# Optimization experiments

Hardware: AMD Instinct MI355X
Metric: run time of the kernel (lower is better)

The kernel has to match this reference:

```python
import jax, jax.numpy as jnp
import numpy as np

NUM_CLASSES = 1203
NO_OBJECT = NUM_CLASSES - 1  # CONSTANTS.NO_OBJECT_LABEL
BZ, N = 64, 100


def _cxcywh_to_xyxy(b):
    cx, cy, w, h = b[..., 0], b[..., 1], b[..., 2], b[..., 3]
    return jnp.stack([cx - w / 2, cy - h / 2, cx + w / 2, cy + h / 2], axis=-1)


def _pairwise_iou_np(a, b):
    # a: [M,4] xyxy, b: [K,4] xyxy -> [M,K]
    area_a = (a[:, 2] - a[:, 0]) * (a[:, 3] - a[:, 1])
    area_b = (b[:, 2] - b[:, 0]) * (b[:, 3] - b[:, 1])
    lt = np.maximum(a[:, None, :2], b[None, :, :2])
    rb = np.minimum(a[:, None, 2:], b[None, :, 2:])
    wh = np.clip(rb - lt, 0.0, None)
    inter = wh[..., 0] * wh[..., 1]
    union = area_a[:, None] + area_b[None, :] - inter
    return inter / np.maximum(union, 1e-9)


def _lsa(cost):
    # Exact Hungarian (Jonker-Volgenant / e-maxx potentials), square cost [n,n].
    # Returns col_of_row: assigned column (target) for each row (prediction).
    n = cost.shape[0]
    INF = 1e18
    u = np.zeros(n + 1)
    v = np.zeros(n + 1)
    p = np.zeros(n + 1, dtype=np.int64)   # p[j] = row matched to column j (1-indexed)
    way = np.zeros(n + 1, dtype=np.int64)
    for i in range(1, n + 1):
        p[0] = i
        j0 = 0
        minv = np.full(n + 1, INF)
        used = np.zeros(n + 1, dtype=bool)
        while True:
            used[j0] = True
            i0 = p[j0]
            cur = cost[i0 - 1] - u[i0] - v[1:]
            unused = ~used[1:]
            improve = unused & (cur < minv[1:])
            minv[1:][improve] = cur[improve]
            way[1:][improve] = j0
            masked = np.where(unused, minv[1:], INF)
            j1 = int(np.argmin(masked)) + 1
            delta = masked[j1 - 1]
            u[p[used]] += delta
            v[used] -= delta
            minv[1:][unused] -= delta
            j0 = j1
            if p[j0] == 0:
                break
        while j0 != 0:
            j1 = way[j0]
            p[j0] = p[j1]
            j0 = j1
    col_of_row = np.zeros(n, dtype=np.int64)
    for j in range(1, n + 1):
        col_of_row[p[j] - 1] = j - 1
    return col_of_row


def _cxcywh_to_xyxy_np(b):
    cx, cy, w, h = b[..., 0], b[..., 1], b[..., 2], b[..., 3]
    return np.stack([cx - w / 2, cy - h / 2, cx + w / 2, cy + h / 2], axis=-1)


def _hungarian_match(labs, lab_preds, bbox, bbox_preds):
    # numpy matcher, mirrors HungarianMatcher.forward (no_grad).
    bz = labs.shape[0]
    # stable softmax over classes
    z = lab_preds - lab_preds.max(axis=-1, keepdims=True)
    e = np.exp(z)
    probs = e / e.sum(axis=-1, keepdims=True)  # [bz,N,C]
    gt_idx = np.zeros(labs.shape, dtype=np.int64)
    for b in range(bz):
        cost_class = -probs[b][:, labs[b]]                                   # [N,N]
        cost_bbox = np.abs(bbox_preds[b][:, None, :] - bbox[b][None, :, :]).sum(-1)
        iou = _pairwise_iou_np(_cxcywh_to_xyxy_np(bbox_preds[b]),
                               _cxcywh_to_xyxy_np(bbox[b]))
        C = cost_class + cost_bbox + (1.0 - iou)
        gt_idx[b] = _lsa(C.astype(np.float64))  # row_ind == arange(N) for square C
    return gt_idx


def _elementwise_iou(a, b):
    # a, b: [...,4] xyxy, paired IoU
    lt = jnp.maximum(a[..., :2], b[..., :2])
    rb = jnp.minimum(a[..., 2:], b[..., 2:])
    wh = jnp.clip(rb - lt, 0.0)
    inter = wh[..., 0] * wh[..., 1]
    area_a = (a[..., 2] - a[..., 0]) * (a[..., 3] - a[..., 1])
    area_b = (b[..., 2] - b[..., 0]) * (b[..., 3] - b[..., 1])
    union = area_a + area_b - inter
    return inter / jnp.maximum(union, 1e-9)


def _detr_loss(labs, lab_preds, bbox, bbox_preds, gt_idx):
    # Re-gather GT by matching (pred side is identity since row_ind=arange(N)).
    new_labs = jnp.take_along_axis(labs, gt_idx, axis=1)                  # [bz,N]
    new_bbox = jnp.take_along_axis(bbox, gt_idx[..., None], axis=1)      # [bz,N,4]
    probs = jax.nn.softmax(lab_preds, axis=-1)
    pred_cls = jnp.argmax(probs, axis=-1)
    mask = (new_labs != NO_OBJECT) & (new_labs == pred_cls)              # [bz,N]
    # classification term: mean over ALL bz*N entries of -p[gt_label]
    loss_label = -jnp.take_along_axis(probs, new_labs[..., None], axis=2).squeeze(-1)
    loss_label = loss_label.mean()
    cnt = mask.sum()
    # L1: torch's bbox[mask] flattens -> .sum(-1).mean() is a plain SUM of |diff|
    l1 = jnp.sum(jnp.abs(new_bbox - bbox_preds) * mask[..., None])
    # IoU loss: mean over masked boxes of (1 - iou)
    iou = _elementwise_iou(_cxcywh_to_xyxy(new_bbox), _cxcywh_to_xyxy(bbox_preds))
    liou = jnp.sum((1.0 - iou) * mask) / jnp.maximum(cnt, 1)
    return loss_label + l1 + liou


def setup_inputs() -> dict:
    key = jax.random.key(0)
    k1, k2, k3, k4 = jax.random.split(key, 4)
    labs = jax.random.randint(k1, (BZ, N), 0, NUM_CLASSES, dtype=jnp.int64)
    lab_preds = jax.random.normal(k2, (BZ, N, NUM_CLASSES), dtype=jnp.float32)
    bbox = jax.random.uniform(k3, (BZ, N, 4), dtype=jnp.float32)
    bbox_preds = jax.random.uniform(k4, (BZ, N, 4), dtype=jnp.float32)
    return {"labs": labs, "lab_preds": lab_preds, "bbox": bbox, "bbox_preds": bbox_preds}


def reference(labs, lab_preds, bbox, bbox_preds):
    gt_idx = _hungarian_match(np.asarray(labs),
                              np.asarray(lab_preds, dtype=np.float64),
                              np.asarray(bbox, dtype=np.float64),
                              np.asarray(bbox_preds, dtype=np.float64))
    return _detr_loss(labs, lab_preds, bbox, bbox_preds, jnp.asarray(gt_idx))
```

## Files before the change

### kernel.cpp

```cpp
#include <hip/hip_runtime.h>
#include <hip/hip_bf16.h>
#include <math.h>
#include <float.h>

#define BZ 64
#define NQ 100
#define NCLS 1203
#define NO_OBJ 1202
constexpr double HUNG_INF = 1e18;
#define KINF 0xC3ABC16D674EC800ull

__device__ inline double readlane_f64(double x, int l) {
  int lo = __builtin_amdgcn_readlane(__double2loint(x), l);
  int hi = __builtin_amdgcn_readlane(__double2hiint(x), l);
  return __hiloint2double(hi, lo);
}

template <int CTRL>
__device__ inline unsigned dpp_mov_u32(unsigned x) {
  return (unsigned)__builtin_amdgcn_update_dpp((int)x, (int)x, CTRL, 0xF, 0xF, false);
}
__device__ inline unsigned umin32(unsigned a, unsigned b) { return a < b ? a : b; }

__device__ inline unsigned wave_min_u32(unsigned x) {
  x = umin32(x, dpp_mov_u32<0xB1>(x));
  x = umin32(x, dpp_mov_u32<0x4E>(x));
  x = umin32(x, dpp_mov_u32<0x141>(x));
  x = umin32(x, dpp_mov_u32<0x128>(x));
  unsigned a = (unsigned)__builtin_amdgcn_readlane((int)x, 0);
  unsigned c = (unsigned)__builtin_amdgcn_readlane((int)x, 16);
  unsigned d = (unsigned)__builtin_amdgcn_readlane((int)x, 32);
  unsigned e = (unsigned)__builtin_amdgcn_readlane((int)x, 48);
  return umin32(umin32(a, c), umin32(d, e));
}

__device__ inline unsigned long long f64_key(double d) {
  long long b = __double_as_longlong(d);
  long long m = (b >> 63) | (long long)0x8000000000000000ll;
  return (unsigned long long)(b ^ m);
}
__device__ inline double key_to_f64(unsigned long long k) {
  long long kk = (long long)k;
  long long m = ((~kk) >> 63) | (long long)0x8000000000000000ll;
  return __longlong_as_double(kk ^ m);
}

__global__ __launch_bounds__(64) void rowstats_kernel(
    const float* __restrict__ lab_preds,
    double* __restrict__ rowmax, double* __restrict__ rowsum,
    float* __restrict__ mxf, float* __restrict__ sf, int* __restrict__ amx) {
  const int r = blockIdx.x;
  const int t = threadIdx.x;
  const float* row = lab_preds + (size_t)r * NCLS;
  float fm = -FLT_MAX; int am = NCLS;
  for (int c = t; c < NCLS; c += 64) {
    float vv = row[c];
    if (vv > fm) { fm = vv; am = c; }
  }
#pragma unroll
  for (int off = 32; off; off >>= 1) {
    float ov = __shfl_xor(fm, off); int oi = __shfl_xor(am, off);
    if (ov > fm || (ov == fm && oi < am)) { fm = ov; am = oi; }
  }
  const double mx = (double)fm;
  double s = 0.0;
  for (int c = t; c < NCLS; c += 64) s += exp((double)row[c] - mx);
#pragma unroll
  for (int off = 32; off; off >>= 1) s += __shfl_xor(s, off);
  float sfl = 0.0f;
  for (int c = t; c < NCLS; c += 64) sfl += expf(row[c] - fm);
#pragma unroll
  for (int off = 32; off; off >>= 1) sfl += __shfl_xor(sfl, off);
  if (t == 0) {
    rowmax[r] = mx; rowsum[r] = s;
    mxf[r] = fm; sf[r] = sfl; amx[r] = am;
  }
}

__global__ __launch_bounds__(64) void match_kernel(
    const int* __restrict__ labs, const float* __restrict__ lab_preds,
    const float* __restrict__ bbox, const float* __restrict__ bbox_preds,
    const double* __restrict__ rowmax, const double* __restrict__ rowsum,
    int* __restrict__ gt_idx) {
  __shared__ double2 Csh2[NQ * 64];
  __shared__ int labs_sh[NQ];
  __shared__ int rowclaim[NQ];
  __shared__ double pxy[NQ][4], txy[NQ][4], pcx[NQ][4], tcx[NQ][4];
  __shared__ double areaP[NQ], areaT[NQ], rmax[NQ], rsum[NQ];

  const int b = blockIdx.x;
  const int lane = threadIdx.x;

  for (int j = lane; j < NQ; j += 64) {
    labs_sh[j] = labs[b * NQ + j];
    const float* tb = bbox + ((size_t)b * NQ + j) * 4;
    double cx = tb[0], cy = tb[1], w = tb[2], h = tb[3];
    tcx[j][0] = cx; tcx[j][1] = cy; tcx[j][2] = w; tcx[j][3] = h;
    double x1 = cx - w * 0.5, y1 = cy - h * 0.5, x2 = cx + w * 0.5, y2 = cy + h * 0.5;
    txy[j][0] = x1; txy[j][1] = y1; txy[j][2] = x2; txy[j][3] = y2;
    areaT[j] = (x2 - x1) * (y2 - y1);
    const float* pb = bbox_preds + ((size_t)b * NQ + j) * 4;
    cx = pb[0]; cy = pb[1]; w = pb[2]; h = pb[3];
    pcx[j][0] = cx; pcx[j][1] = cy; pcx[j][2] = w; pcx[j][3] = h;
    x1 = cx - w * 0.5; y1 = cy - h * 0.5; x2 = cx + w * 0.5; y2 = cy + h * 0.5;
    pxy[j][0] = x1; pxy[j][1] = y1; pxy[j][2] = x2; pxy[j][3] = y2;
    areaP[j] = (x2 - x1) * (y2 - y1);
    rmax[j] = rowmax[b * NQ + j];
    rsum[j] = rowsum[b * NQ + j];
  }
  for (int r = lane; r < NQ; r += 64) rowclaim[r] = -1;
  __syncthreads();

  for (int i = 0; i < NQ; ++i) {
    double cA, cB = 0.0;
    {
      const int j = lane;
      double pc = exp((double)lab_preds[((size_t)b * NQ + i) * NCLS + labs_sh[j]] - rmax[i]) / rsum[i];
      double cb = fabs(pcx[i][0] - tcx[j][0]) + fabs(pcx[i][1] - tcx[j][1])
                + fabs(pcx[i][2] - tcx[j][2]) + fabs(pcx[i][3] - tcx[j][3]);
      double ltx = fmax(pxy[i][0], txy[j][0]);
      double lty = fmax(pxy[i][1], txy[j][1]);
      double rbx = fmin(pxy[i][2], txy[j][2]);
      double rby = fmin(pxy[i][3], txy[j][3]);
      double inter = fmax(rbx - ltx, 0.0) * fmax(rby - lty, 0.0);
      double uni = areaP[i] + areaT[j] - inter;
      double iou = inter / fmax(uni, 1e-9);
      cA = -pc + cb + (1.0 - iou);
    }
    if (lane + 64 < NQ) {
      const int j = lane + 64;
      double pc = exp((double)lab_preds[((size_t)b * NQ + i) * NCLS + labs_sh[j]] - rmax[i]) / rsum[i];
      double cb = fabs(pcx[i][0] - tcx[j][0]) + fabs(pcx[i][1] - tcx[j][1])
                + fabs(pcx[i][2] - tcx[j][2]) + fabs(pcx[i][3] - tcx[j][3]);
      double ltx = fmax(pxy[i][0], txy[j][0]);
      double lty = fmax(pxy[i][1], txy[j][1]);
      double rbx = fmin(pxy[i][2], txy[j][2]);
      double rby = fmin(pxy[i][3], txy[j][3]);
      double inter = fmax(rbx - ltx, 0.0) * fmax(rby - lty, 0.0);
      double uni = areaP[i] + areaT[j] - inter;
      double iou = inter / fmax(uni, 1e-9);
      cB = -pc + cb + (1.0 - iou);
    }
    Csh2[i * 64 + lane] = make_double2(cA, cB);
  }
  __syncthreads();

  const bool has1 = (lane + 65 <= NQ);

  double mn0 = DBL_MAX, mn1 = DBL_MAX; int ar0 = 0, ar1 = 0;
  for (int i = 0; i < NQ; ++i) {
    double2 cd = Csh2[i * 64 + lane];
    if (cd.x < mn0) { mn0 = cd.x; ar0 = i; }
    if (has1 && cd.y < mn1) { mn1 = cd.y; ar1 = i; }
  }
  double v0 = mn0, v1 = has1 ? mn1 : 0.0;
  double u0 = 0.0, u1 = 0.0;
  int p0c = 0, p1c = 0;
  if (atomicCAS(&rowclaim[ar0], -1, lane) == -1) p0c = ar0 + 1;
  if (has1 && atomicCAS(&rowclaim[ar1], -1, 64 + lane) == -1) p1c = ar1 + 1;
  __syncthreads();

  int cl0 = rowclaim[lane];
  unsigned long long fm0 = __ballot(cl0 == -1);
  int cl1 = (lane < NQ - 64) ? rowclaim[64 + lane] : 0;
  unsigned long long fm1 = __ballot((lane < NQ - 64) && cl1 == -1);

  while (fm0 | fm1) {
    int f;
    if (fm0) { f = (int)__ffsll(fm0) - 1; fm0 &= fm0 - 1; }
    else     { f = 64 + (int)__ffsll(fm1) - 1; fm1 &= fm1 - 1; }
    const int fi = f + 1;

    double minv0 = HUNG_INF, minv1 = HUNG_INF;
    int way0 = 0, way1 = 0;
    bool used0 = false, used1 = false;
    double u_i = 0.0;
    int j0 = 0, i0 = fi;
    double ui0 = 0.0;
    double2 cd = Csh2[(i0 - 1) * 64 + lane];
    while (true) {
      if (j0 == lane + 1) used0 = true;
      if (j0 == lane + 65) used1 = true;

      const double c0 = cd.x;
      const double c1 = cd.y;

      if (!used0) {
        double cur = (c0 - ui0) - v0;
        if (cur < minv0) { minv0 = cur; way0 = j0; }
      }
      if (has1 && !used1) {
        double cur = (c1 - ui0) - v1;
        if (cur < minv1) { minv1 = cur; way1 = j0; }
      }
      const unsigned long long k0 = used0 ? KINF : f64_key(minv0);
      const unsigned long long k1 = has1 ? (used1 ? KINF : f64_key(minv1)) : ~0ull;

      const unsigned h0 = (unsigned)(k0 >> 32), h1 = (unsigned)(k1 >> 32);
      const unsigned KH = wave_min_u32(umin32(h0, h1));
      unsigned long long blh0 = __ballot(h0 == KH);
      unsigned long long blh1 = __ballot(h1 == KH);
      int j1, lj;
      unsigned long long KEY;
      if (__popcll(blh0) + __popcll(blh1) == 1) {
        if (blh0) {
          lj = (int)__ffsll(blh0) - 1; j1 = lj + 1;
          KEY = ((unsigned long long)KH << 32) |
                (unsigned)__builtin_amdgcn_readlane((int)(unsigned)k0, lj);
        } else {
          lj = (int)__ffsll(blh1) - 1; j1 = lj + 65;
          KEY = ((unsigned long long)KH << 32) |
                (unsigned)__builtin_amdgcn_readlane((int)(unsigned)k1, lj);
        }
      } else {
        const unsigned lo0 = (h0 == KH) ? (unsigned)k0 : 0xFFFFFFFFu;
        const unsigned lo1 = (h1 == KH) ? (unsigned)k1 : 0xFFFFFFFFu;
        const unsigned KL = wave_min_u32(umin32(lo0, lo1));
        KEY = ((unsigned long long)KH << 32) | KL;
        unsigned long long bl0 = __ballot(k0 == KEY);
        if (bl0) { lj = (int)__ffsll(bl0) - 1; j1 = lj + 1; }
        else {
          unsigned long long bl1 = __ballot(k1 == KEY);
          lj = (int)__ffsll(bl1) - 1; j1 = lj + 65;
        }
      }

      int pj1; double uj1;
      if (j1 <= 64) { pj1 = __builtin_amdgcn_readlane(p0c, lj); uj1 = readlane_f64(u0, lj); }
      else          { pj1 = __builtin_amdgcn_readlane(p1c, lj); uj1 = readlane_f64(u1, lj); }
      const int nrow = (pj1 > 0 ? pj1 : 1) - 1;
      double2 cd_next = Csh2[nrow * 64 + lane];

      const double delta = key_to_f64(KEY);
      if (used0)        { v0 -= delta; u0 += delta; }
      else              { minv0 -= delta; }
      if (has1) {
        if (used1)      { v1 -= delta; u1 += delta; }
        else            { minv1 -= delta; }
      }
      u_i += delta;

      j0 = j1; i0 = pj1; ui0 = uj1; cd = cd_next;
      if (pj1 == 0) break;
    }
    int jj = j0;
    while (jj != 0) {
      int ljj = (jj <= 64) ? (jj - 1) : (jj - 65);
      int jn = (jj <= 64) ? __builtin_amdgcn_readlane(way0, ljj)
                          : __builtin_amdgcn_readlane(way1, ljj);
      int pn; double un;
      if (jn == 0) { pn = fi; un = u_i; }
      else {
        int ln = (jn <= 64) ? (jn - 1) : (jn - 65);
        if (jn <= 64) { pn = __builtin_amdgcn_readlane(p0c, ln); un = readlane_f64(u0, ln); }
        else          { pn = __builtin_amdgcn_readlane(p1c, ln); un = readlane_f64(u1, ln); }
      }
      if (jj == lane + 1)  { p0c = pn; u0 = un; }
      if (jj == lane + 65) { p1c = pn; u1 = un; }
      jj = jn;
    }
  }

  gt_idx[b * NQ + p0c - 1] = lane;
  if (has1) gt_idx[b * NQ + p1c - 1] = lane + 64;
}

__global__ __launch_bounds__(256) void lossfinal_kernel(
    const int* __restrict__ labs, const float* __restrict__ lab_preds,
    const float* __restrict__ bbox, const float* __restrict__ bbox_preds,
    const int* __restrict__ gt_idx,
    const float* __restrict__ mxf, const float* __restrict__ sf,
    const int* __restrict__ amx,
    double* __restrict__ acc, int* __restrict__ cnt_out) {
  const int r = blockIdx.x * 256 + threadIdx.x;
  double lab_t = 0.0, l1_t = 0.0, iou_t = 0.0;
  int c_t = 0;
  if (r < BZ * NQ) {
    const int b = r / NQ;
    const int g = gt_idx[r];
    const int nl = labs[b * NQ + g];
    const float val = lab_preds[(size_t)r * NCLS + nl];
    const float pg = expf(val - mxf[r]) / sf[r];
    lab_t = -(double)pg;
    if (nl != NO_OBJ && nl == amx[r]) {
      c_t = 1;
      const float* pb = bbox_preds + (size_t)r * 4;
      const float* tb = bbox + ((size_t)b * NQ + g) * 4;
      float l1 = fabsf(tb[0] - pb[0]) + fabsf(tb[1] - pb[1])
               + fabsf(tb[2] - pb[2]) + fabsf(tb[3] - pb[3]);
      l1_t = (double)l1;
      float px1 = pb[0] - pb[2] * 0.5f, py1 = pb[1] - pb[3] * 0.5f;
      float px2 = pb[0] + pb[2] * 0.5f, py2 = pb[1] + pb[3] * 0.5f;
      float tx1 = tb[0] - tb[2] * 0.5f, ty1 = tb[1] - tb[3] * 0.5f;
      float tx2 = tb[0] + tb[2] * 0.5f, ty2 = tb[1] + tb[3] * 0.5f;
      float ltx = fmaxf(px1, tx1), lty = fmaxf(py1, ty1);
      float rbx = fminf(px2, tx2), rby = fminf(py2, ty2);
      float inter = fmaxf(rbx - ltx, 0.0f) * fmaxf(rby - lty, 0.0f);
      float uni = (px2 - px1) * (py2 - py1) + (tx2 - tx1) * (ty2 - ty1) - inter;
      float iou = inter / fmaxf(uni, 1e-9f);
      iou_t = (double)(1.0f - iou);
    }
  }
#pragma unroll
  for (int off = 32; off; off >>= 1) {
    lab_t += __shfl_xor(lab_t, off);
    l1_t  += __shfl_xor(l1_t, off);
    iou_t += __shfl_xor(iou_t, off);
    c_t   += __shfl_xor(c_t, off);
  }
  __shared__ double s_lab[4], s_l1[4], s_iou[4];
  __shared__ int s_cnt[4];
  const int wave = threadIdx.x >> 6;
  if ((threadIdx.x & 63) == 0) { s_lab[wave] = lab_t; s_l1[wave] = l1_t; s_iou[wave] = iou_t; s_cnt[wave] = c_t; }
  __syncthreads();
  if (threadIdx.x == 0) {
    double a = 0.0, bb = 0.0, c = 0.0; int n = 0;
    for (int w = 0; w < 4; ++w) { a += s_lab[w]; bb += s_l1[w]; c += s_iou[w]; n += s_cnt[w]; }
    atomicAdd(&acc[0], a);
    atomicAdd(&acc[1], bb);
    atomicAdd(&acc[2], c);
    atomicAdd(cnt_out, n);
  }
}

__global__ void finalize_kernel(const double* __restrict__ acc, const int* __restrict__ cnt,
                                float* __restrict__ out) {
  int n = *cnt; if (n < 1) n = 1;
  out[0] = (float)(acc[0] / (double)(BZ * NQ) + acc[1] + acc[2] / (double)n);
}

extern "C" void kernel_launch(void* const* d_in, const int* in_sizes, int n_in,
                              void* d_out, int out_size, void* d_ws, size_t ws_size,
                              hipStream_t stream) {
  const int*   labs       = (const int*)d_in[0];
  const float* lab_preds  = (const float*)d_in[1];
  const float* bbox       = (const float*)d_in[2];
  const float* bbox_preds = (const float*)d_in[3];

  char* ws = (char*)d_ws;
  int*    gt_idx = (int*)ws;
  double* acc    = (double*)(ws + 25600);
  int*    cnt    = (int*)(ws + 25624);
  double* rowmax = (double*)(ws + 25632);
  double* rowsum = (double*)(ws + 76832);
  float*  mxf    = (float*)(ws + 128032);
  float*  sfw    = (float*)(ws + 153632);
  int*    amx    = (int*)(ws + 179232);

  hipMemsetAsync(ws + 25600, 0, 32, stream);
  rowstats_kernel<<<BZ * NQ, 64, 0, stream>>>(lab_preds, rowmax, rowsum, mxf, sfw, amx);
  match_kernel<<<BZ, 64, 0, stream>>>(labs, lab_preds, bbox, bbox_preds, rowmax, rowsum, gt_idx);
  lossfinal_kernel<<<(BZ * NQ + 255) / 256, 256, 0, stream>>>(
      labs, lab_preds, bbox, bbox_preds, gt_idx, mxf, sfw, amx, acc, cnt);
  finalize_kernel<<<1, 1, 0, stream>>>(acc, cnt, (float*)d_out);
}
```

Baseline: 514.1 us.

## Add augmenting row-reduction passes before Hungarian shortest-path augmentation

Adds two Jonker-Volgenant style augmenting row-reduction passes after the column-reduction initial assignment. Each free row finds its two smallest reduced costs with 64-bit wave min reductions, claims the best column, adjusts that column's potential and may evict the previous owner. The goal is to shrink the number of free rows left for the costly shortest-path augmentation loop. In exchange it adds extra wave reductions per free row, and the potentials must stay consistent for exactness.

```diff
diff --git a/kernel.cpp b/kernel.cpp
--- a/kernel.cpp
+++ b/kernel.cpp
@@ -32,6 +32,14 @@
   unsigned d = (unsigned)__builtin_amdgcn_readlane((int)x, 32);
   unsigned e = (unsigned)__builtin_amdgcn_readlane((int)x, 48);
   return umin32(umin32(a, c), umin32(d, e));
+}
+
+__device__ inline unsigned long long wave_min_u64(unsigned long long k) {
+  unsigned h = (unsigned)(k >> 32);
+  unsigned KH = wave_min_u32(h);
+  unsigned lo = (h == KH) ? (unsigned)k : 0xFFFFFFFFu;
+  unsigned KL = wave_min_u32(lo);
+  return ((unsigned long long)KH << 32) | KL;
 }
 
 __device__ inline unsigned long long f64_key(double d) {
@@ -164,6 +172,47 @@
   unsigned long long fm0 = __ballot(cl0 == -1);
   int cl1 = (lane < NQ - 64) ? rowclaim[64 + lane] : 0;
   unsigned long long fm1 = __ballot((lane < NQ - 64) && cl1 == -1);
+
+  for (int pass = 0; pass < 2; ++pass) {
+    unsigned long long todo0 = fm0, todo1 = fm1;
+    while (todo0 | todo1) {
+      int f;
+      if (todo0) { f = (int)__ffsll(todo0) - 1; todo0 &= todo0 - 1; }
+      else       { f = 64 + (int)__ffsll(todo1) - 1; todo1 &= todo1 - 1; }
+      double2 cf = Csh2[f * 64 + lane];
+      unsigned long long k0 = f64_key(cf.x - v0);
+      unsigned long long k1 = has1 ? f64_key(cf.y - v1) : ~0ull;
+      unsigned long long K1 = wave_min_u64(k0 < k1 ? k0 : k1);
+      unsigned long long bl0 = __ballot(k0 == K1);
+      int lj, slot;
+      if (bl0) { lj = (int)__ffsll(bl0) - 1; slot = 0; }
+      else { unsigned long long bl1 = __ballot(k1 == K1); lj = (int)__ffsll(bl1) - 1; slot = 1; }
+      unsigned long long k0b = (slot == 0 && lane == lj) ? ~0ull : k0;
+      unsigned long long k1b = (slot == 1 && lane == lj) ? ~0ull : k1;
+      unsigned long long K2 = wave_min_u64(k0b < k1b ? k0b : k1b);
+      const double m2 = key_to_f64(K2);
+      int i1 = (slot == 0) ? __builtin_amdgcn_readlane(p0c, lj)
+                           : __builtin_amdgcn_readlane(p1c, lj);
+      if (K1 < K2) {
+        double dm = m2 - key_to_f64(K1);
+        if (slot == 0 && lane == lj) v0 -= dm;
+        if (slot == 1 && lane == lj) v1 -= dm;
+      } else if (i1 != 0) {
+        unsigned long long bl0b = __ballot(k0b == K2);
+        if (bl0b) { lj = (int)__ffsll(bl0b) - 1; slot = 0; }
+        else { unsigned long long bl1b = __ballot(k1b == K2); lj = (int)__ffsll(bl1b) - 1; slot = 1; }
+        i1 = (slot == 0) ? __builtin_amdgcn_readlane(p0c, lj)
+                         : __builtin_amdgcn_readlane(p1c, lj);
+      }
+      if (slot == 0 && lane == lj) { p0c = f + 1; u0 = m2; }
+      if (slot == 1 && lane == lj) { p1c = f + 1; u1 = m2; }
+      if (f < 64) fm0 &= ~(1ull << f); else fm1 &= ~(1ull << (f - 64));
+      if (i1 != 0) {
+        int k = i1 - 1;
+        if (k < 64) fm0 |= (1ull << k); else fm1 |= (1ull << (k - 64));
+      }
+    }
+  }
 
   while (fm0 | fm1) {
     int f;
```

Measured after the change: 494.7 us. 1.04x faster.
